# Kernel tuning notes

Hardware: AMD Instinct MI355X
Metric: run time of the kernel (lower is better)

Reference implementation:

```python
import jax, jax.numpy as jnp
import numpy as np

EPS = 1e-7  # tf.keras.backend.epsilon()
ROUTINGS = 3


def setup_inputs() -> dict:
    key = jax.random.key(0)
    k1, k2 = jax.random.split(key)
    x = jax.random.normal(k1, (64, 2048, 8), dtype=jnp.float32)
    W = jax.random.normal(k2, (32, 2048, 16, 8), dtype=jnp.float32) * 0.05
    return {"x": x, "W": W}


def _squash(s):
    # source squash: vectors / sqrt(sum(v^2) + eps)
    ssq = jnp.sum(s * s, axis=-1, keepdims=True)
    return s / jnp.sqrt(ssq + EPS)


def reference(x, W):
    # x: [B, N, I]; W: [J, N, D, I]
    # prediction vectors u_hat: [B, J, N, D]
    u_hat = jnp.einsum('bni,jndi->bjnd', x, W)
    b = jnp.zeros(u_hat.shape[:-1], dtype=u_hat.dtype)  # [B, J, N]
    v = None
    for i in range(ROUTINGS):
        c = jax.nn.softmax(b, axis=1)                       # coupling over output caps J
        s = jnp.einsum('bjnd,bjn->bjd', u_hat, c)           # weighted sum over input caps N
        v = _squash(s)                                      # [B, J, D]
        if i < ROUTINGS - 1:
            b = b + jnp.einsum('bjnd,bjd->bjn', u_hat, v)   # agreement update
    return v
```

## Files before the change

kernel.cpp:

```cpp
#include <hip/hip_runtime.h>


#define BB_ 64
#define NN_ 2048
#define II_ 8
#define JJ_ 32
#define DD_ 16
#define NCHUNKS 64
#define CHUNK 32
#define BG 8
#define NBG (BB_ / BG)
#define EPS_ 1e-7f

#define PARTIAL_FLOATS (NCHUNKS * BB_ * JJ_ * DD_)

typedef __attribute__((ext_vector_type(2))) float v2f;

template <int CTRL>
__device__ __forceinline__ float dpp_add(float v) {
  const int s = __builtin_amdgcn_update_dpp(
      0, __builtin_bit_cast(int, v), CTRL, 0xf, 0xf, true);
  return v + __builtin_bit_cast(float, s);
}
#define DPP_QP_XOR1 0xB1
#define DPP_QP_XOR2 0x4E
#define DPP_HALF_MIRROR 0x141
#define DPP_ROR8 0x128

struct W8 {
  v2f k[8];
};

__device__ __forceinline__ W8 loadW(const float* p) {
  const float4* q = (const float4*)p;
  const float4 t0 = q[0], t1 = q[1], t2 = q[2], t3 = q[3];
  W8 w = {{{t0.x, t2.x}, {t0.y, t2.y},
           {t0.z, t2.z}, {t0.w, t2.w},
           {t1.x, t3.x}, {t1.y, t3.y},
           {t1.z, t3.z}, {t1.w, t3.w}}};
  return w;
}

__device__ __forceinline__ void compute_u(const W8& w, const float* __restrict__ x,
                                          int b0, int n, v2f (&u)[BG]) {
#pragma unroll
  for (int b = 0; b < BG; ++b) {
    const float4* __restrict__ xr =
        (const float4*)(x + ((size_t)(b0 + b) * NN_ + n) * II_);
    const float4 xa = xr[0];
    const float4 xb = xr[1];
    v2f acc = w.k[0] * xa.x;
    acc += w.k[1] * xa.y;
    acc += w.k[2] * xa.z;
    acc += w.k[3] * xa.w;
    acc += w.k[4] * xb.x;
    acc += w.k[5] * xb.y;
    acc += w.k[6] * xb.z;
    acc += w.k[7] * xb.w;
    u[b] = acc;
  }
}

template <int PHASE>
__global__ __launch_bounds__(256, 4) void caps_phase(
    const float* __restrict__ x, const float* __restrict__ W,
    const float* __restrict__ V, float* __restrict__ partial) {
  const int tid = threadIdx.x;
  const int j = tid >> 3;
  const int p = tid & 7;
  const int chunk = blockIdx.x & (NCHUNKS - 1);
  const int bg = blockIdx.x / NCHUNKS;
  const int b0 = bg * BG;
  const int n0 = chunk * CHUNK;

  __shared__ float lmat[BG][JJ_];
  __shared__ float cmat[BG][JJ_];

  const float* wp = W + (size_t)j * (NN_ * DD_ * II_) +
                    (size_t)n0 * (DD_ * II_) + (size_t)p * 16;

  float v0r[BG], v1r[BG];
  if (PHASE > 0) {
#pragma unroll
    for (int b = 0; b < BG; ++b) {
      const float2 vv =
          *(const float2*)&V[((size_t)(b0 + b) * JJ_ + j) * DD_ + 2 * p];
      v0r[b] = vv.x;
      v1r[b] = vv.y;
    }
  }

  v2f s[BG];
#pragma unroll
  for (int b = 0; b < BG; ++b) s[b] = (v2f)(0.f);

  W8 wc = loadW(wp);

  for (int nl = 0; nl < CHUNK; ++nl) {
    const int n = n0 + nl;
    const int nf = (nl + 1 < CHUNK) ? nl + 1 : nl;
    const W8 wn = loadW(wp + (size_t)nf * 128);

    v2f u[BG];
    compute_u(wc, x, b0, n, u);

    if (PHASE == 0) {
#pragma unroll
      for (int b = 0; b < BG; ++b) s[b] += u[b];
    } else {
#pragma unroll
      for (int b = 0; b < BG; ++b) {
        float lp = u[b].x * v0r[b] + u[b].y * v1r[b];
        lp = dpp_add<DPP_QP_XOR1>(lp);
        lp = dpp_add<DPP_QP_XOR2>(lp);
        lp = dpp_add<DPP_HALF_MIRROR>(lp);
        if (p == 0) lmat[b][j] = lp;
      }
      __syncthreads();
      {
        const int jj = tid & 31;
        const int bb = tid >> 5;
        float e0 = __expf(lmat[bb][jj]);
        float m0 = e0;
        m0 = dpp_add<DPP_QP_XOR1>(m0);
        m0 = dpp_add<DPP_QP_XOR2>(m0);
        m0 = dpp_add<DPP_HALF_MIRROR>(m0);
        m0 = dpp_add<DPP_ROR8>(m0);
        m0 += __shfl_xor(m0, 16);
        cmat[bb][jj] = e0 * __builtin_amdgcn_rcpf(m0);
      }
      __syncthreads();
#pragma unroll
      for (int b = 0; b < BG; ++b) {
        const float c = cmat[b][j];
        s[b] += u[b] * c;
      }
    }
    wc = wn;
  }

  const float scale = (PHASE == 0) ? (1.0f / 32.0f) : 1.0f;
#pragma unroll
  for (int b = 0; b < BG; ++b) {
    const size_t off =
        ((size_t)chunk * BB_ + (b0 + b)) * (JJ_ * DD_) + j * DD_ + 2 * p;
    *(float2*)&partial[off] = make_float2(s[b].x * scale, s[b].y * scale);
  }
}

template <int MODE>
__global__ __launch_bounds__(128) void caps_reduce(
    const float* __restrict__ partial, float* __restrict__ V,
    float* __restrict__ out) {
  const int t = blockIdx.x * 128 + threadIdx.x;
  float s = 0.f;
#pragma unroll 8
  for (int c = 0; c < NCHUNKS; ++c)
    s += partial[(size_t)c * (BB_ * JJ_ * DD_) + t];
  float ss = s * s;
  ss += __shfl_xor(ss, 1);
  ss += __shfl_xor(ss, 2);
  ss += __shfl_xor(ss, 4);
  ss += __shfl_xor(ss, 8);
  const float v = s / sqrtf(ss + EPS_);
  if (MODE == 0)
    V[t] = v;
  else if (MODE == 1)
    V[t] += v;
  else
    out[t] = v;
}

extern "C" void kernel_launch(void* const* d_in, const int* in_sizes, int n_in,
                              void* d_out, int out_size, void* d_ws,
                              size_t ws_size, hipStream_t stream) {
  const float* x = (const float*)d_in[0];
  const float* W = (const float*)d_in[1];
  float* out = (float*)d_out;
  float* partial = (float*)d_ws;
  float* V = partial + PARTIAL_FLOATS;

  const dim3 kgrid(NBG * NCHUNKS);
  const dim3 rgrid((BB_ * JJ_ * DD_) / 128);

  caps_phase<0><<<kgrid, 256, 0, stream>>>(x, W, nullptr, partial);
  caps_reduce<0><<<rgrid, 128, 0, stream>>>(partial, V, out);
  caps_phase<1><<<kgrid, 256, 0, stream>>>(x, W, V, partial);
  caps_reduce<1><<<rgrid, 128, 0, stream>>>(partial, V, out);
  caps_phase<2><<<kgrid, 256, 0, stream>>>(x, W, V, partial);
  caps_reduce<2><<<rgrid, 128, 0, stream>>>(partial, V, out);
}
```

Measured before the change: 194.9 us.

## Halve chunk size, double-buffer W prefetch two steps ahead, widen reduce blocks

```diff
diff --git a/kernel.cpp b/kernel.cpp
--- a/kernel.cpp
+++ b/kernel.cpp
@@ -6,8 +6,8 @@
 #define II_ 8
 #define JJ_ 32
 #define DD_ 16
-#define NCHUNKS 64
-#define CHUNK 32
+#define NCHUNKS 128
+#define CHUNK 16
 #define BG 8
 #define NBG (BB_ / BG)
 #define EPS_ 1e-7f
@@ -27,36 +27,42 @@
 #define DPP_HALF_MIRROR 0x141
 #define DPP_ROR8 0x128
 
-struct W8 {
-  v2f k[8];
+struct Wraw {
+  float4 q[4];
 };
 
-__device__ __forceinline__ W8 loadW(const float* p) {
+__device__ __forceinline__ Wraw loadWraw(const float* p) {
   const float4* q = (const float4*)p;
-  const float4 t0 = q[0], t1 = q[1], t2 = q[2], t3 = q[3];
-  W8 w = {{{t0.x, t2.x}, {t0.y, t2.y},
-           {t0.z, t2.z}, {t0.w, t2.w},
-           {t1.x, t3.x}, {t1.y, t3.y},
-           {t1.z, t3.z}, {t1.w, t3.w}}};
+  Wraw w;
+  w.q[0] = q[0];
+  w.q[1] = q[1];
+  w.q[2] = q[2];
+  w.q[3] = q[3];
   return w;
 }
 
-__device__ __forceinline__ void compute_u(const W8& w, const float* __restrict__ x,
-                                          int b0, int n, v2f (&u)[BG]) {
+__device__ __forceinline__ void compute_u(const Wraw& w,
+                                          const float* __restrict__ x, int b0,
+                                          int n, v2f (&u)[BG]) {
+  const float4 t0 = w.q[0], t1 = w.q[1], t2 = w.q[2], t3 = w.q[3];
+  const v2f k0 = {t0.x, t2.x}, k1 = {t0.y, t2.y};
+  const v2f k2 = {t0.z, t2.z}, k3 = {t0.w, t2.w};
+  const v2f k4 = {t1.x, t3.x}, k5 = {t1.y, t3.y};
+  const v2f k6 = {t1.z, t3.z}, k7 = {t1.w, t3.w};
 #pragma unroll
   for (int b = 0; b < BG; ++b) {
     const float4* __restrict__ xr =
         (const float4*)(x + ((size_t)(b0 + b) * NN_ + n) * II_);
     const float4 xa = xr[0];
     const float4 xb = xr[1];
-    v2f acc = w.k[0] * xa.x;
-    acc += w.k[1] * xa.y;
-    acc += w.k[2] * xa.z;
-    acc += w.k[3] * xa.w;
-    acc += w.k[4] * xb.x;
-    acc += w.k[5] * xb.y;
-    acc += w.k[6] * xb.z;
-    acc += w.k[7] * xb.w;
+    v2f acc = k0 * xa.x;
+    acc += k1 * xa.y;
+    acc += k2 * xa.z;
+    acc += k3 * xa.w;
+    acc += k4 * xb.x;
+    acc += k5 * xb.y;
+    acc += k6 * xb.z;
+    acc += k7 * xb.w;
     u[b] = acc;
   }
 }
@@ -69,7 +75,7 @@
   const int j = tid >> 3;
   const int p = tid & 7;
   const int chunk = blockIdx.x & (NCHUNKS - 1);
-  const int bg = blockIdx.x / NCHUNKS;
+  const int bg = blockIdx.x >> 7;
   const int b0 = bg * BG;
   const int n0 = chunk * CHUNK;
 
@@ -94,49 +100,86 @@
 #pragma unroll
   for (int b = 0; b < BG; ++b) s[b] = (v2f)(0.f);
 
-  W8 wc = loadW(wp);
-
-  for (int nl = 0; nl < CHUNK; ++nl) {
-    const int n = n0 + nl;
-    const int nf = (nl + 1 < CHUNK) ? nl + 1 : nl;
-    const W8 wn = loadW(wp + (size_t)nf * 128);
-
-    v2f u[BG];
-    compute_u(wc, x, b0, n, u);
-
-    if (PHASE == 0) {
-#pragma unroll
-      for (int b = 0; b < BG; ++b) s[b] += u[b];
-    } else {
-#pragma unroll
-      for (int b = 0; b < BG; ++b) {
-        float lp = u[b].x * v0r[b] + u[b].y * v1r[b];
-        lp = dpp_add<DPP_QP_XOR1>(lp);
-        lp = dpp_add<DPP_QP_XOR2>(lp);
-        lp = dpp_add<DPP_HALF_MIRROR>(lp);
-        if (p == 0) lmat[b][j] = lp;
-      }
-      __syncthreads();
-      {
-        const int jj = tid & 31;
-        const int bb = tid >> 5;
-        float e0 = __expf(lmat[bb][jj]);
-        float m0 = e0;
-        m0 = dpp_add<DPP_QP_XOR1>(m0);
-        m0 = dpp_add<DPP_QP_XOR2>(m0);
-        m0 = dpp_add<DPP_HALF_MIRROR>(m0);
-        m0 = dpp_add<DPP_ROR8>(m0);
-        m0 += __shfl_xor(m0, 16);
-        cmat[bb][jj] = e0 * __builtin_amdgcn_rcpf(m0);
-      }
-      __syncthreads();
-#pragma unroll
-      for (int b = 0; b < BG; ++b) {
-        const float c = cmat[b][j];
-        s[b] += u[b] * c;
+  Wraw wA = loadWraw(wp);
+  Wraw wB = loadWraw(wp + 128);
+
+  for (int nl = 0; nl < CHUNK; nl += 2) {
+    const int nf2 = (nl + 2 < CHUNK) ? nl + 2 : CHUNK - 1;
+    const int nf3 = (nl + 3 < CHUNK) ? nl + 3 : CHUNK - 1;
+    const Wraw tA = loadWraw(wp + (size_t)nf2 * 128);
+
+    {
+      v2f u[BG];
+      compute_u(wA, x, b0, n0 + nl, u);
+      if (PHASE == 0) {
+#pragma unroll
+        for (int b = 0; b < BG; ++b) s[b] += u[b];
+      } else {
+#pragma unroll
+        for (int b = 0; b < BG; ++b) {
+          float lp = u[b].x * v0r[b] + u[b].y * v1r[b];
+          lp = dpp_add<DPP_QP_XOR1>(lp);
+          lp = dpp_add<DPP_QP_XOR2>(lp);
+          lp = dpp_add<DPP_HALF_MIRROR>(lp);
+          if (p == 0) lmat[b][j] = lp;
+        }
+        __syncthreads();
+        {
+          const int jj = tid & 31;
+          const int bb = tid >> 5;
+          float e0 = __expf(lmat[bb][jj]);
+          float m0 = e0;
+          m0 = dpp_add<DPP_QP_XOR1>(m0);
+          m0 = dpp_add<DPP_QP_XOR2>(m0);
+          m0 = dpp_add<DPP_HALF_MIRROR>(m0);
+          m0 = dpp_add<DPP_ROR8>(m0);
+          m0 += __shfl_xor(m0, 16);
+          cmat[bb][jj] = e0 * __builtin_amdgcn_rcpf(m0);
+        }
+        __syncthreads();
+#pragma unroll
+        for (int b = 0; b < BG; ++b) s[b] += u[b] * cmat[b][j];
       }
     }
-    wc = wn;
+
+    const Wraw tB = loadWraw(wp + (size_t)nf3 * 128);
+
+    {
+      v2f u[BG];
+      compute_u(wB, x, b0, n0 + nl + 1, u);
+      if (PHASE == 0) {
+#pragma unroll
+        for (int b = 0; b < BG; ++b) s[b] += u[b];
+      } else {
+#pragma unroll
+        for (int b = 0; b < BG; ++b) {
+          float lp = u[b].x * v0r[b] + u[b].y * v1r[b];
+          lp = dpp_add<DPP_QP_XOR1>(lp);
+          lp = dpp_add<DPP_QP_XOR2>(lp);
+          lp = dpp_add<DPP_HALF_MIRROR>(lp);
+          if (p == 0) lmat[b][j] = lp;
+        }
+        __syncthreads();
+        {
+          const int jj = tid & 31;
+          const int bb = tid >> 5;
+          float e0 = __expf(lmat[bb][jj]);
+          float m0 = e0;
+          m0 = dpp_add<DPP_QP_XOR1>(m0);
+          m0 = dpp_add<DPP_QP_XOR2>(m0);
+          m0 = dpp_add<DPP_HALF_MIRROR>(m0);
+          m0 = dpp_add<DPP_ROR8>(m0);
+          m0 += __shfl_xor(m0, 16);
+          cmat[bb][jj] = e0 * __builtin_amdgcn_rcpf(m0);
+        }
+        __syncthreads();
+#pragma unroll
+        for (int b = 0; b < BG; ++b) s[b] += u[b] * cmat[b][j];
+      }
+    }
+
+    wA = tA;
+    wB = tB;
   }
 
   const float scale = (PHASE == 0) ? (1.0f / 32.0f) : 1.0f;
@@ -149,12 +192,12 @@
 }
 
 template <int MODE>
-__global__ __launch_bounds__(128) void caps_reduce(
+__global__ __launch_bounds__(256) void caps_reduce(
     const float* __restrict__ partial, float* __restrict__ V,
     float* __restrict__ out) {
-  const int t = blockIdx.x * 128 + threadIdx.x;
+  const int t = blockIdx.x * 256 + threadIdx.x;
   float s = 0.f;
-#pragma unroll 8
+#pragma unroll 16
   for (int c = 0; c < NCHUNKS; ++c)
     s += partial[(size_t)c * (BB_ * JJ_ * DD_) + t];
   float ss = s * s;
@@ -181,12 +224,12 @@
   float* V = partial + PARTIAL_FLOATS;
 
   const dim3 kgrid(NBG * NCHUNKS);
-  const dim3 rgrid((BB_ * JJ_ * DD_) / 128);
+  const dim3 rgrid((BB_ * JJ_ * DD_) / 256);
 
   caps_phase<0><<<kgrid, 256, 0, stream>>>(x, W, nullptr, partial);
-  caps_reduce<0><<<rgrid, 128, 0, stream>>>(partial, V, out);
+  caps_reduce<0><<<rgrid, 256, 0, stream>>>(partial, V, out);
   caps_phase<1><<<kgrid, 256, 0, stream>>>(x, W, V, partial);
-  caps_reduce<1><<<rgrid, 128, 0, stream>>>(partial, V, out);
+  caps_reduce<1><<<rgrid, 256, 0, stream>>>(partial, V, out);
   caps_phase<2><<<kgrid, 256, 0, stream>>>(x, W, V, partial);
-  caps_reduce<2><<<rgrid, 128, 0, stream>>>(partial, V, out);
-}
+  caps_reduce<2><<<rgrid, 256, 0, stream>>>(partial, V, out);
+}
```

Result: slower. 277.1 us (+42.2%).
